# Performance work log

Hardware: AMD Instinct MI355X
Metric: run time of the kernel (lower is better)

Reference implementation:

```python
import jax, jax.numpy as jnp
import numpy as np

IN_FEATURES = 4096
OUT_FEATURES = 4096
BINS = 65536
TOKENS = 8192


def setup_inputs() -> dict:
    key = jax.random.key(0)
    k_x, k_w, k_b, k_idx = jax.random.split(key, 4)
    bound = 1.0 / np.sqrt(OUT_FEATURES)
    x = jax.random.normal(k_x, (TOKENS, IN_FEATURES), dtype=jnp.float32)
    weight = jax.random.uniform(k_w, (BINS,), dtype=jnp.float32, minval=-bound, maxval=bound)
    bias = jax.random.uniform(k_b, (OUT_FEATURES,), dtype=jnp.float32, minval=-bound, maxval=bound)
    indices_hash = jax.random.randint(k_idx, (OUT_FEATURES * IN_FEATURES,), 0, BINS, dtype=jnp.int32)
    return {"x": x, "weight": weight, "bias": bias, "indices_hash": indices_hash}


def reference(x, weight, bias, indices_hash):
    # Reconstruct dense weight [out, in] by gathering from the shared bins.
    true_weight = jnp.take(weight, indices_hash, axis=0).reshape(OUT_FEATURES, IN_FEATURES)
    # F.linear: x @ W^T + b
    return jnp.einsum("ti,oi->to", x, true_weight) + bias
```

## Files before the change

### kernel.cpp

```cpp
#include <hip/hip_runtime.h>
#include <hip/hip_bf16.h>

#define TOKENS 8192
#define NOUT   4096
#define KIN    4096

typedef __attribute__((ext_vector_type(8))) short short8;
typedef __attribute__((ext_vector_type(4))) float f32x4;

__device__ __forceinline__ short f2bf(float f) {
  union { float f; unsigned u; } v; v.f = f;
  unsigned r = v.u + 0x7fffu + ((v.u >> 16) & 1u);
  return (short)(r >> 16);
}

__device__ __forceinline__ void async_copy16(const void* g, void* l) {
  __builtin_amdgcn_global_load_lds(
      (const __attribute__((address_space(1))) void*)g,
      (__attribute__((address_space(3))) void*)l, 16, 0, 0);
}

__global__ void pack_w_kernel(const int4* __restrict__ idx,
                              const float* __restrict__ w,
                              short8* __restrict__ wb) {
  size_t t = (size_t)blockIdx.x * blockDim.x + threadIdx.x;
  int4 a = idx[2 * t];
  int4 b = idx[2 * t + 1];
  short8 o;
  o[0] = f2bf(w[a.x]); o[1] = f2bf(w[a.y]);
  o[2] = f2bf(w[a.z]); o[3] = f2bf(w[a.w]);
  o[4] = f2bf(w[b.x]); o[5] = f2bf(w[b.y]);
  o[6] = f2bf(w[b.z]); o[7] = f2bf(w[b.w]);
  wb[t] = o;
}

__global__ void pack_x_kernel(const float4* __restrict__ x,
                              short8* __restrict__ xb) {
  size_t t = (size_t)blockIdx.x * blockDim.x + threadIdx.x;
  float4 a = x[2 * t];
  float4 b = x[2 * t + 1];
  short8 o;
  o[0] = f2bf(a.x); o[1] = f2bf(a.y); o[2] = f2bf(a.z); o[3] = f2bf(a.w);
  o[4] = f2bf(b.x); o[5] = f2bf(b.y); o[6] = f2bf(b.z); o[7] = f2bf(b.w);
  xb[t] = o;
}

#define BM 128
#define BN 128
#define BK 32

__global__ void gemm_kernel(const short* __restrict__ A,
                            const short* __restrict__ B,
                            const float* __restrict__ bias,
                            float* __restrict__ C) {
  __shared__ __align__(128) short As[BM * BK];
  __shared__ __align__(128) short Bs[BN * BK];

  const int tid  = threadIdx.x;
  const int lane = tid & 63;
  const int wave = tid >> 6;
  const int wr = wave >> 1;
  const int wc = wave & 1;

  const int nwg = gridDim.x;
  const int cpx = nwg >> 3;
  const int b   = blockIdx.x;
  const int swz = (b & 7) * cpx + (b >> 3);
  const int bm  = swz & 63;
  const int bn  = swz >> 6;

  const short* a_base = A + (size_t)(bm * BM) * KIN;
  const short* b_base = B + (size_t)(bn * BN) * KIN;

  f32x4 acc[4][4] = {};

  const int sr = tid >> 2;
  const int sc = (tid & 3) * 8;

  for (int k0 = 0; k0 < KIN; k0 += BK) {
    __syncthreads();
    async_copy16(a_base + (size_t)sr * KIN + k0 + sc,        &As[sr * BK + sc]);
    async_copy16(a_base + (size_t)(sr + 64) * KIN + k0 + sc, &As[(sr + 64) * BK + sc]);
    async_copy16(b_base + (size_t)sr * KIN + k0 + sc,        &Bs[sr * BK + sc]);
    async_copy16(b_base + (size_t)(sr + 64) * KIN + k0 + sc, &Bs[(sr + 64) * BK + sc]);
    __syncthreads();

    const int kg   = (lane >> 4) * 8;
    const int arow = wr * 64 + (lane & 15);
    const int bcol = wc * 64 + (lane & 15);
    short8 af[4], bfr[4];
#pragma unroll
    for (int m = 0; m < 4; ++m)
      af[m] = *(const short8*)&As[(arow + m * 16) * BK + kg];
#pragma unroll
    for (int n = 0; n < 4; ++n)
      bfr[n] = *(const short8*)&Bs[(bcol + n * 16) * BK + kg];
#pragma unroll
    for (int m = 0; m < 4; ++m)
#pragma unroll
      for (int n = 0; n < 4; ++n)
        acc[m][n] = __builtin_amdgcn_mfma_f32_16x16x32_bf16(af[m], bfr[n], acc[m][n], 0, 0, 0);
  }

  const int crow0 = bm * BM + wr * 64 + (lane >> 4) * 4;
  const int ccol0 = bn * BN + wc * 64 + (lane & 15);
  float bs[4];
#pragma unroll
  for (int n = 0; n < 4; ++n) bs[n] = bias[ccol0 + n * 16];
#pragma unroll
  for (int m = 0; m < 4; ++m) {
#pragma unroll
    for (int j = 0; j < 4; ++j) {
      float* crow = C + (size_t)(crow0 + m * 16 + j) * NOUT;
#pragma unroll
      for (int n = 0; n < 4; ++n)
        crow[ccol0 + n * 16] = acc[m][n][j] + bs[n];
    }
  }
}

extern "C" void kernel_launch(void* const* d_in, const int* in_sizes, int n_in,
                              void* d_out, int out_size, void* d_ws, size_t ws_size,
                              hipStream_t stream) {
  const float* x      = (const float*)d_in[0];
  const float* weight = (const float*)d_in[1];
  const float* bias   = (const float*)d_in[2];
  const int*   idx    = (const int*)d_in[3];
  float* out = (float*)d_out;

  short* wb = (short*)d_ws;
  short* xb = (short*)((char*)d_ws + (size_t)NOUT * KIN * sizeof(short));

  pack_w_kernel<<<((size_t)NOUT * KIN) / (8 * 256), 256, 0, stream>>>(
      (const int4*)idx, weight, (short8*)wb);
  pack_x_kernel<<<((size_t)TOKENS * KIN) / (8 * 256), 256, 0, stream>>>(
      (const float4*)x, (short8*)xb);
  gemm_kernel<<<(TOKENS / BM) * (NOUT / BN), 256, 0, stream>>>(xb, wb, bias, out);
}
```

Before: 674.8 us.

## Rewrite GEMM as 256x256 double-buffered pipelined tile with swizzled LDS

```diff
diff --git a/kernel.cpp b/kernel.cpp
--- a/kernel.cpp
+++ b/kernel.cpp
@@ -45,76 +45,131 @@
   xb[t] = o;
 }
 
-#define BM 128
-#define BN 128
-#define BK 32
+#define BM 256
+#define BN 256
+#define BK 64
+#define NT    (KIN / BK)
+#define NITER (NT / 2)
 
-__global__ void gemm_kernel(const short* __restrict__ A,
-                            const short* __restrict__ B,
-                            const float* __restrict__ bias,
-                            float* __restrict__ C) {
-  __shared__ __align__(128) short As[BM * BK];
-  __shared__ __align__(128) short Bs[BN * BK];
+#define BARX()  __builtin_amdgcn_s_barrier()
+#define FENCE() __builtin_amdgcn_sched_barrier(0)
+#define WAITVM(N) asm volatile("s_waitcnt vmcnt(" #N ")" ::: "memory")
+
+__global__ __launch_bounds__(512, 2) void gemm_kernel(const short* __restrict__ A,
+                                                      const short* __restrict__ B,
+                                                      const float* __restrict__ bias,
+                                                      float* __restrict__ C) {
+  __shared__ short As[2][BM * BK];
+  __shared__ short Bs[2][BN * BK];
 
   const int tid  = threadIdx.x;
   const int lane = tid & 63;
   const int wave = tid >> 6;
-  const int wr = wave >> 1;
-  const int wc = wave & 1;
+  const int wr = wave >> 2;
+  const int wc = wave & 3;
 
-  const int nwg = gridDim.x;
-  const int cpx = nwg >> 3;
   const int b   = blockIdx.x;
-  const int swz = (b & 7) * cpx + (b >> 3);
-  const int bm  = swz & 63;
-  const int bn  = swz >> 6;
+  const int swz = (b & 7) * 64 + (b >> 3);
+  const int bm  = swz & 31;
+  const int bn  = swz >> 5;
 
-  const short* a_base = A + (size_t)(bm * BM) * KIN;
-  const short* b_base = B + (size_t)(bn * BN) * KIN;
+  const int srow = tid >> 3;
+  const int sch  = ((tid & 7) ^ (srow & 7)) * 8;
+  const short* aS = A + (size_t)(bm * 256 + srow) * KIN + sch;
+  const short* bS = B + (size_t)(bn * 256 + srow) * KIN + sch;
+  short* aD0 = &As[0][tid * 8];
+  short* aD1 = &As[1][tid * 8];
+  short* bD0 = &Bs[0][tid * 8];
+  short* bD1 = &Bs[1][tid * 8];
 
-  f32x4 acc[4][4] = {};
+#define STG_A(BUF, BLK, T) async_copy16(aS + (size_t)(BLK) * 64 * KIN + (size_t)(T) * 64, \
+                                        ((BUF) ? aD1 : aD0) + (BLK) * 4096)
+#define STG_B(BUF, BLK, T) async_copy16(bS + (size_t)(BLK) * 64 * KIN + (size_t)(T) * 64, \
+                                        ((BUF) ? bD1 : bD0) + (BLK) * 4096)
 
-  const int sr = tid >> 2;
-  const int sc = (tid & 3) * 8;
+  const int l15   = lane & 15;
+  const int sw    = (l15 & 7) << 4;
+  const int lanek = (lane >> 4) * 16;
+  int csw[2];
+  csw[0] = (0  + lanek) ^ sw;
+  csw[1] = (64 + lanek) ^ sw;
+  const int aBase = (wr * 128 + l15) * 128;
+  const int bBase = (wc * 64  + l15) * 128;
 
-  for (int k0 = 0; k0 < KIN; k0 += BK) {
-    __syncthreads();
-    async_copy16(a_base + (size_t)sr * KIN + k0 + sc,        &As[sr * BK + sc]);
-    async_copy16(a_base + (size_t)(sr + 64) * KIN + k0 + sc, &As[(sr + 64) * BK + sc]);
-    async_copy16(b_base + (size_t)sr * KIN + k0 + sc,        &Bs[sr * BK + sc]);
-    async_copy16(b_base + (size_t)(sr + 64) * KIN + k0 + sc, &Bs[(sr + 64) * BK + sc]);
-    __syncthreads();
+  short8 af[4][2];
+  short8 bfr[2][2][2];
+  f32x4 acc[8][4] = {};
 
-    const int kg   = (lane >> 4) * 8;
-    const int arow = wr * 64 + (lane & 15);
-    const int bcol = wc * 64 + (lane & 15);
-    short8 af[4], bfr[4];
-#pragma unroll
-    for (int m = 0; m < 4; ++m)
-      af[m] = *(const short8*)&As[(arow + m * 16) * BK + kg];
-#pragma unroll
-    for (int n = 0; n < 4; ++n)
-      bfr[n] = *(const short8*)&Bs[(bcol + n * 16) * BK + kg];
-#pragma unroll
-    for (int m = 0; m < 4; ++m)
-#pragma unroll
-      for (int n = 0; n < 4; ++n)
-        acc[m][n] = __builtin_amdgcn_mfma_f32_16x16x32_bf16(af[m], bfr[n], acc[m][n], 0, 0, 0);
+#define RD_A(BUF, MH) { const char* _p = (const char*)((BUF) ? As[1] : As[0]) + aBase + (MH) * 8192; \
+  _Pragma("unroll") for (int mf = 0; mf < 4; ++mf) \
+  _Pragma("unroll") for (int ks = 0; ks < 2; ++ks) \
+    af[mf][ks] = *(const short8*)(_p + mf * 2048 + csw[ks]); }
+
+#define RD_B(BUF, NH) { const char* _p = (const char*)((BUF) ? Bs[1] : Bs[0]) + bBase + (NH) * 4096; \
+  _Pragma("unroll") for (int nf = 0; nf < 2; ++nf) \
+  _Pragma("unroll") for (int ks = 0; ks < 2; ++ks) \
+    bfr[NH][nf][ks] = *(const short8*)(_p + nf * 2048 + csw[ks]); }
+
+#define MM(MH, NH) { __builtin_amdgcn_s_setprio(1); \
+  _Pragma("unroll") for (int mf = 0; mf < 4; ++mf) \
+  _Pragma("unroll") for (int nf = 0; nf < 2; ++nf) \
+  _Pragma("unroll") for (int ks = 0; ks < 2; ++ks) \
+    acc[(MH) * 4 + mf][(NH) * 2 + nf] = __builtin_amdgcn_mfma_f32_16x16x32_bf16( \
+        af[mf][ks], bfr[NH][nf][ks], acc[(MH) * 4 + mf][(NH) * 2 + nf], 0, 0, 0); \
+  __builtin_amdgcn_s_setprio(0); }
+
+  STG_A(0, 0, 0); STG_A(0, 1, 0); STG_A(0, 2, 0); STG_A(0, 3, 0);
+  STG_B(0, 0, 0); STG_B(0, 1, 0); STG_B(0, 2, 0); STG_B(0, 3, 0);
+  STG_A(1, 0, 1); STG_A(1, 2, 1);
+  WAITVM(2); FENCE(); BARX();
+
+  for (int it = 0; it < NITER; ++it) {
+    const int t1  = 2 * it + 1;
+    const int tn0 = 2 * it + 2;
+    const int tn1 = 2 * it + 3;
+    const bool pf = (it < NITER - 1);
+
+    RD_A(0, 0); RD_B(0, 0);
+    STG_A(1, 1, t1); STG_A(1, 3, t1);
+    BARX(); MM(0, 0); BARX();
+    RD_B(0, 1);
+    STG_B(1, 0, t1); STG_B(1, 1, t1);
+    BARX(); MM(0, 1); BARX();
+    RD_A(0, 1);
+    STG_B(1, 2, t1); STG_B(1, 3, t1);
+    BARX(); MM(1, 0); BARX();
+    if (pf) { STG_A(0, 0, tn0); STG_A(0, 2, tn0); }
+    BARX(); MM(1, 1);
+    if (pf) { WAITVM(2); } else { WAITVM(0); }
+    FENCE(); BARX();
+
+    RD_A(1, 0); RD_B(1, 0);
+    if (pf) { STG_A(0, 1, tn0); STG_A(0, 3, tn0); }
+    BARX(); MM(0, 0); BARX();
+    RD_B(1, 1);
+    if (pf) { STG_B(0, 0, tn0); STG_B(0, 1, tn0); }
+    BARX(); MM(0, 1); BARX();
+    RD_A(1, 1);
+    if (pf) { STG_B(0, 2, tn0); STG_B(0, 3, tn0); }
+    BARX(); MM(1, 0); BARX();
+    if (pf) { STG_A(1, 0, tn1); STG_A(1, 2, tn1); }
+    BARX(); MM(1, 1);
+    WAITVM(2); FENCE(); BARX();
   }
 
-  const int crow0 = bm * BM + wr * 64 + (lane >> 4) * 4;
-  const int ccol0 = bn * BN + wc * 64 + (lane & 15);
-  float bs[4];
+  const int crow0 = bm * 256 + wr * 128 + (lane >> 4) * 4;
+  const int ccol0 = bn * 256 + wc * 64 + l15;
+  float bsv[4];
 #pragma unroll
-  for (int n = 0; n < 4; ++n) bs[n] = bias[ccol0 + n * 16];
+  for (int nf = 0; nf < 4; ++nf) bsv[nf] = bias[ccol0 + nf * 16];
 #pragma unroll
-  for (int m = 0; m < 4; ++m) {
+  for (int mf = 0; mf < 8; ++mf) {
 #pragma unroll
     for (int j = 0; j < 4; ++j) {
-      float* crow = C + (size_t)(crow0 + m * 16 + j) * NOUT;
+      float* cr = C + (size_t)(crow0 + mf * 16 + j) * NOUT;
 #pragma unroll
-      for (int n = 0; n < 4; ++n)
-        crow[ccol0 + n * 16] = acc[m][n][j] + bs[n];
+      for (int nf = 0; nf < 4; ++nf)
+        cr[ccol0 + nf * 16] = acc[mf][nf][j] + bsv[nf];
     }
   }
 }
@@ -135,5 +190,5 @@
       (const int4*)idx, weight, (short8*)wb);
   pack_x_kernel<<<((size_t)TOKENS * KIN) / (8 * 256), 256, 0, stream>>>(
       (const float4*)x, (short8*)xb);
-  gemm_kernel<<<(TOKENS / BM) * (NOUT / BN), 256, 0, stream>>>(xb, wb, bias, out);
+  gemm_kernel<<<(TOKENS / BM) * (NOUT / BN), 512, 0, stream>>>(xb, wb, bias, out);
 }
```

Result: faster. 590.9 us (-12.4%).
